# Performance work log

Measured on AMD Instinct MI355X. Metric: run time of the kernel, lower is better.

The kernel has to match this reference:

```python
import jax, jax.numpy as jnp
import numpy as np

B, S, F = 256, 192, 64
HD, L, PRED = 1024, 2, 48


def setup_inputs() -> dict:
    key = jax.random.key(0)
    ks = jax.random.split(key, 9)
    s_in = 1.0 / np.sqrt(F)
    s_h = 1.0 / np.sqrt(HD)
    return {
        "x": jax.random.normal(ks[0], (B, S, F), dtype=jnp.float32),
        "W_hidden": jax.random.uniform(ks[1], (F, HD), jnp.float32, -s_in, s_in),
        "b_hidden": jax.random.uniform(ks[2], (HD,), jnp.float32, -s_in, s_in),
        "Wih": jax.random.uniform(ks[3], (L, HD, HD), jnp.float32, -s_h, s_h),
        "Whh": jax.random.uniform(ks[4], (L, HD, HD), jnp.float32, -s_h, s_h),
        "bih": jax.random.uniform(ks[5], (L, HD), jnp.float32, -s_h, s_h),
        "bhh": jax.random.uniform(ks[6], (L, HD), jnp.float32, -s_h, s_h),
        "Wo": jax.random.uniform(ks[7], (HD, F), jnp.float32, -s_h, s_h),
        "bo": jax.random.uniform(ks[8], (F,), jnp.float32, -s_h, s_h),
    }


def reference(x, W_hidden, b_hidden, Wih, Whh, bih, bhh, Wo, bo):
    # x: [B, S, F]
    x_concat = x @ W_hidden + b_hidden          # [B, S, HD]
    xs = jnp.swapaxes(x_concat, 0, 1)           # [S, B, HD] for time scan
    h0 = jnp.zeros((L, x.shape[0], HD), x.dtype)

    def step(h, x_t):
        # h: [L, B, HD], x_t: [B, HD]; standard tanh-RNN stacked layers
        inp = x_t
        new_h = []
        for l in range(L):
            hl = jnp.tanh(inp @ Wih[l] + bih[l] + h[l] @ Whh[l] + bhh[l])
            new_h.append(hl)
            inp = hl
        h_new = jnp.stack(new_h)
        return h_new, h_new[-1]

    _, ys = jax.lax.scan(step, h0, xs)           # ys: [S, B, HD] top-layer states
    # torch code stores h for t in [0, S-2] only (drops last timestep)
    H = jnp.swapaxes(ys[:-1], 0, 1)              # [B, S-1, HD]
    H = jax.nn.relu(H)
    out = H @ Wo + bo                            # [B, S-1, F]
    return out[:, -PRED:, :]
```

## Files before the change

kernel.cpp:

```cpp
#include <hip/hip_runtime.h>
#include <hip/hip_bf16.h>

#define B    256
#define S    192
#define F    64
#define HD   1024
#define PRED 48
#define TSTART (S - 1 - PRED)
#define NSLOT 48

typedef __attribute__((ext_vector_type(8))) short short8;
typedef __attribute__((ext_vector_type(4))) float f32x4;
typedef unsigned int u32;

static __device__ __forceinline__ short f2bf(float f) {
    __hip_bfloat16 h = __float2bfloat16(f);
    return *reinterpret_cast<short*>(&h);
}
static __device__ __forceinline__ f32x4 mfma16(short8 a, short8 b, f32x4 c) {
    return __builtin_amdgcn_mfma_f32_16x16x32_bf16(a, b, c, 0, 0, 0);
}
static __device__ __forceinline__ short8 ld8(const short* p) {
    return *reinterpret_cast<const short8*>(p);
}
static __device__ __forceinline__ void st_state(short* p, short v) {
    __hip_atomic_store(p, v, __ATOMIC_RELAXED, __HIP_MEMORY_SCOPE_AGENT);
}
static __device__ __forceinline__ u32 ld_flag(const u32* p) {
    return __hip_atomic_load(p, __ATOMIC_RELAXED, __HIP_MEMORY_SCOPE_AGENT);
}
static __device__ __forceinline__ void st_flag(u32* p, u32 v) {
    __hip_atomic_store(p, v, __ATOMIC_RELAXED, __HIP_MEMORY_SCOPE_AGENT);
}

__global__ void fold_kernel(const float* __restrict__ Wh,
                            const float* __restrict__ Wih0,
                            float* __restrict__ Wfold) {
    const int n = (blockIdx.x & 3) * 256 + threadIdx.x;
    const int f = blockIdx.x >> 2;
    float a = 0.f;
#pragma unroll 16
    for (int k = 0; k < HD; ++k)
        a += Wh[f * HD + k] * Wih0[(size_t)k * HD + n];
    Wfold[f * HD + n] = a;
}

__global__ void bias_kernel(const float* __restrict__ bh,
                            const float* __restrict__ Wih0,
                            const float* __restrict__ bih,
                            const float* __restrict__ bhh,
                            float* __restrict__ bf0,
                            float* __restrict__ bf1) {
    __shared__ float red[256];
    const int nl = threadIdx.x & 15;
    const int kc = threadIdx.x >> 4;
    const int n  = blockIdx.x * 16 + nl;
    float a = 0.f;
#pragma unroll 8
    for (int k = kc * 64; k < kc * 64 + 64; ++k)
        a += bh[k] * Wih0[(size_t)k * HD + n];
    red[threadIdx.x] = a;
    __syncthreads();
    if (kc == 0) {
        float s = 0.f;
#pragma unroll
        for (int j = 0; j < 16; ++j) s += red[j * 16 + nl];
        bf0[n] = s + bih[n] + bhh[n];
        bf1[n] = bih[HD + n] + bhh[HD + n];
    }
}

__global__ void transpose_cast(const float* __restrict__ src,
                               short* __restrict__ dst, int K, int N) {
    __shared__ float tile[64][65];
    const int nk = K >> 6;
    const int bk = blockIdx.x % nk;
    const int bn = blockIdx.x / nk;
    const int i  = threadIdx.x;
    {
        const int c4 = (i & 15) * 4;
        for (int it = 0; it < 4; ++it) {
            const int k = (i >> 4) + it * 16;
            const float4 v = *reinterpret_cast<const float4*>(
                &src[(size_t)(bk * 64 + k) * N + bn * 64 + c4]);
            tile[k][c4 + 0] = v.x; tile[k][c4 + 1] = v.y;
            tile[k][c4 + 2] = v.z; tile[k][c4 + 3] = v.w;
        }
    }
    __syncthreads();
    {
        const int n  = i >> 2;
        const int kb = (i & 3) * 16;
        short* dp = &dst[(size_t)(bn * 64 + n) * K + bk * 64 + kb];
#pragma unroll
        for (int j = 0; j < 16; ++j) dp[j] = f2bf(tile[kb + j][n]);
    }
}

__global__ void xcast(const float* __restrict__ x, short* __restrict__ xb) {
    const size_t i = ((size_t)blockIdx.x * 256 + threadIdx.x) * 4;
    const float4 v = *reinterpret_cast<const float4*>(&x[i]);
    short4 o;
    o.x = f2bf(v.x); o.y = f2bf(v.y); o.z = f2bf(v.z); o.w = f2bf(v.w);
    *reinterpret_cast<short4*>(&xb[i]) = o;
}

static __device__ __forceinline__ void stage1(char* lds, const short* __restrict__ src,
                                              int row0) {
    const int tid = threadIdx.x;
#pragma unroll
    for (int it = 0; it < 8; ++it) {
        const int idx = it * 512 + tid;
        const int r   = (idx >> 2) & 31;
        const int off = ((idx >> 7) << 6) + ((idx & 3) << 4);
        const f32x4 v = *reinterpret_cast<const f32x4*>(
            (const char*)src + (size_t)(row0 + r) * 2048 + off);
        *reinterpret_cast<f32x4*>(lds + (idx << 4)) = v;
    }
}

static __device__ __forceinline__ void stage2(char* lds,
                                              const short* __restrict__ s0,
                                              const short* __restrict__ s1,
                                              int row0) {
    const int tid = threadIdx.x;
#pragma unroll
    for (int it = 0; it < 8; ++it) {
        const int idx = it * 512 + tid;
        const int r   = (idx >> 2) & 31;
        const int off = ((idx >> 7) << 6) + ((idx & 3) << 4);
        const size_t g = (size_t)(row0 + r) * 2048 + off;
        const f32x4 a = *reinterpret_cast<const f32x4*>((const char*)s0 + g);
        const f32x4 b = *reinterpret_cast<const f32x4*>((const char*)s1 + g);
        *reinterpret_cast<f32x4*>(lds + (idx << 4)) = a;
        *reinterpret_cast<f32x4*>(lds + 65536 + (idx << 4)) = b;
    }
}

static __device__ __forceinline__ f32x4 gemmLG(const char* ldsA,
                                               const short* __restrict__ bp,
                                               f32x4 acc_in) {
    f32x4 acc0 = acc_in, acc1 = {0.f,0.f,0.f,0.f};
    short8 b0[8], b1[8];
#pragma unroll
    for (int j = 0; j < 8; ++j) b0[j] = ld8(bp + j * 32);
#pragma unroll
    for (int c = 0; c < 4; ++c) {
        if (c < 3) {
            short8* nxt = (c & 1) ? b0 : b1;
#pragma unroll
            for (int j = 0; j < 8; ++j) nxt[j] = ld8(bp + (c + 1) * 256 + j * 32);
        }
        const short8* cur = (c & 1) ? b1 : b0;
#pragma unroll
        for (int j = 0; j < 8; ++j) {
            const short8 a = *reinterpret_cast<const short8*>(
                ldsA + (c * 8 + j) * 2048);
            if (j & 1) acc1 = mfma16(a, cur[j], acc1);
            else       acc0 = mfma16(a, cur[j], acc0);
        }
    }
    return acc0 + acc1;
}

__global__ __launch_bounds__(512, 1) void rnn_pers(
    const short* __restrict__ xbf,
    const short* __restrict__ WfoldT, const float* __restrict__ bf0,
    const short* __restrict__ WhhT0, const short* __restrict__ WihT1,
    const short* __restrict__ WhhT1, const float* __restrict__ bf1,
    short* h0h, short* h1h, u32* flags0, u32* flags1) {

    extern __shared__ char lds[];

    const int bid   = blockIdx.x;
    const int xcd   = bid & 7;
    const int u     = bid >> 3;
    const int layer = u & 1;
    const int rt    = ((xcd & 3) << 1) | ((u >> 1) & 1);
    const int ct    = ((xcd >> 2) << 3) | ((u >> 2) & 7);
    const int w     = threadIdx.x >> 6;
    const int mh    = w & 1;
    const int nq    = w >> 1;
    const int l     = threadIdx.x & 63;
    const int lr    = l & 15, kg = l >> 4;
    const int row0  = rt * 32;
    const int m0    = row0 + mh * 16;
    const int n0    = ct * 64 + nq * 16;
    const int col   = n0 + lr;
    const int rb    = m0 + kg * 4;
    const char* ldsA = lds + mh * 1024 + lr * 64 + kg * 16;

    const float bb = (layer ? bf1 : bf0)[col];
    u32* myflag = (layer ? flags1 : flags0) + (rt * 16 + ct) * 32;
    const int tid = threadIdx.x;

    if (layer == 0) {
        const short* wf = WfoldT + (size_t)col * F + kg * 8;
        const short8 wf0 = ld8(wf), wf1 = ld8(wf + 32);
        for (int k = 0; k < S - 1; ++k) {
            const short* xp = xbf + ((size_t)(m0 + lr) * S + k) * F + kg * 8;
            const short8 xa0 = ld8(xp);
            const short8 xa1 = ld8(xp + 32);
            if (k > 0) {
                __syncthreads();
                if (tid < 16) {
                    const u32* f = flags0 + (rt * 16 + tid) * 32;
                    while (ld_flag(f) < (u32)k) __builtin_amdgcn_s_sleep(1);
                } else if (tid < 32 && k >= 46) {
                    const u32* f = flags1 + (rt * 16 + (tid - 16)) * 32;
                    while (ld_flag(f) < (u32)(k - 45)) __builtin_amdgcn_s_sleep(1);
                }
                __syncthreads();
                stage1(lds, h0h + (size_t)((k - 1) % NSLOT) * B * HD, row0);
                __syncthreads();
            }
            f32x4 acc = {0.f, 0.f, 0.f, 0.f};
            acc = mfma16(xa0, wf0, acc);
            acc = mfma16(xa1, wf1, acc);
            if (k > 0)
                acc = gemmLG(ldsA, WhhT0 + (size_t)col * HD + kg * 8, acc);
            short* hd = h0h + (size_t)(k % NSLOT) * B * HD;
#pragma unroll
            for (int r = 0; r < 4; ++r)
                st_state(&hd[(size_t)(rb + r) * HD + col],
                         f2bf(tanhf(acc[r] + bb)));
            __syncthreads();
            if (tid == 0) st_flag(myflag, (u32)(k + 1));
        }
    } else {
        if (tid == 0) st_flag(myflag, 1u);
        for (int k = 1; k < S; ++k) {
            const int t = k - 1;
            __syncthreads();
            if (tid < 16) {
                const u32* f = flags0 + (rt * 16 + tid) * 32;
                while (ld_flag(f) < (u32)k) __builtin_amdgcn_s_sleep(1);
            } else if (tid < 32) {
                const u32* f = flags1 + (rt * 16 + (tid - 16)) * 32;
                while (ld_flag(f) < (u32)k) __builtin_amdgcn_s_sleep(1);
            }
            __syncthreads();
            const short* h0src = h0h + (size_t)((k - 1) % NSLOT) * B * HD;
            if (t > 0) {
                stage2(lds, h0src,
                       h1h + (size_t)((t - 1) % NSLOT) * B * HD, row0);
            } else {
                stage1(lds, h0src, row0);
            }
            __syncthreads();
            f32x4 acc = {0.f, 0.f, 0.f, 0.f};
            acc = gemmLG(ldsA, WihT1 + (size_t)col * HD + kg * 8, acc);
            if (t > 0)
                acc = gemmLG(ldsA + 65536, WhhT1 + (size_t)col * HD + kg * 8, acc);
#pragma unroll
            for (int r = 0; r < 4; ++r)
                st_state(&h1h[(size_t)(t % NSLOT) * B * HD
                              + (size_t)(rb + r) * HD + col],
                         f2bf(tanhf(acc[r] + bb)));
            __syncthreads();
            if (tid == 0) st_flag(myflag, (u32)(k + 1));
        }
    }
}

__global__ __launch_bounds__(256) void outgemm(
    const short* __restrict__ h1h, const short* __restrict__ WoT,
    const float* __restrict__ bo, float* __restrict__ out) {
    const int w = threadIdx.x >> 6, l = threadIdx.x & 63;
    const int lr = l & 15, kg = l >> 4;
    const int m0 = blockIdx.x * 64 + w * 16;
    const int arow = m0 + lr;
    const u32 bidx = (u32)arow / 48u;
    const u32 p    = (u32)arow % 48u;
    const u32 slot = (143u + p) % 48u;

    f32x4 acc[4] = {{0.f,0.f,0.f,0.f},{0.f,0.f,0.f,0.f},
                    {0.f,0.f,0.f,0.f},{0.f,0.f,0.f,0.f}};
    const short* ap = h1h + ((size_t)slot * B + bidx) * HD + kg * 8;
    const short* bp = WoT + (size_t)lr * HD + kg * 8;
#pragma unroll 4
    for (int k0 = 0; k0 < HD; k0 += 32) {
        short8 a = ld8(ap + k0);
#pragma unroll
        for (int j = 0; j < 8; ++j) a[j] = (a[j] < 0) ? (short)0 : a[j];
#pragma unroll
        for (int c = 0; c < 4; ++c)
            acc[c] = mfma16(a, ld8(bp + (size_t)c * 16 * HD + k0), acc[c]);
    }
    const int rb = m0 + kg * 4;
#pragma unroll
    for (int c = 0; c < 4; ++c) {
        const float bbv = bo[c * 16 + lr];
#pragma unroll
        for (int r = 0; r < 4; ++r)
            out[(size_t)(rb + r) * F + c * 16 + lr] = acc[c][r] + bbv;
    }
}

extern "C" void kernel_launch(void* const* d_in, const int* in_sizes, int n_in,
                              void* d_out, int out_size, void* d_ws, size_t ws_size,
                              hipStream_t stream) {
    const float* x   = (const float*)d_in[0];
    const float* Wh  = (const float*)d_in[1];
    const float* bh  = (const float*)d_in[2];
    const float* Wih = (const float*)d_in[3];
    const float* Whh = (const float*)d_in[4];
    const float* bih = (const float*)d_in[5];
    const float* bhh = (const float*)d_in[6];
    const float* Wo  = (const float*)d_in[7];
    const float* bo  = (const float*)d_in[8];
    float* out = (float*)d_out;

    char* p = (char*)d_ws;
    float* Wfold  = (float*)p; p += (size_t)F * HD * 4;
    float* bf0    = (float*)p; p += HD * 4;
    float* bf1    = (float*)p; p += HD * 4;
    short* WfoldT = (short*)p; p += (size_t)HD * F * 2;
    short* WhhT0  = (short*)p; p += (size_t)HD * HD * 2;
    short* WihT1  = (short*)p; p += (size_t)HD * HD * 2;
    short* WhhT1  = (short*)p; p += (size_t)HD * HD * 2;
    short* WoT    = (short*)p; p += (size_t)F * HD * 2;
    short* h0h    = (short*)p; p += (size_t)NSLOT * B * HD * 2;
    short* h1h    = (short*)p; p += (size_t)NSLOT * B * HD * 2;
    short* xbf    = (short*)p; p += (size_t)B * S * F * 2;
    u32*   sync   = (u32*)p;  p += 65536;

    hipMemsetAsync(sync, 0, 65536, stream);

    fold_kernel<<<256, 256, 0, stream>>>(Wh, Wih, Wfold);
    bias_kernel<<<64, 256, 0, stream>>>(bh, Wih, bih, bhh, bf0, bf1);
    transpose_cast<<<16, 256, 0, stream>>>(Wfold, WfoldT, F, HD);
    transpose_cast<<<256, 256, 0, stream>>>(Whh, WhhT0, HD, HD);
    transpose_cast<<<256, 256, 0, stream>>>(Wih + (size_t)HD * HD, WihT1, HD, HD);
    transpose_cast<<<256, 256, 0, stream>>>(Whh + (size_t)HD * HD, WhhT1, HD, HD);
    transpose_cast<<<16, 256, 0, stream>>>(Wo, WoT, HD, F);
    xcast<<<(B * S * F) / (256 * 4), 256, 0, stream>>>(x, xbf);

    u32* flags0 = sync;
    u32* flags1 = sync + 4096;
    void* args[] = {
        (void*)&xbf, (void*)&WfoldT, (void*)&bf0, (void*)&WhhT0,
        (void*)&WihT1, (void*)&WhhT1, (void*)&bf1,
        (void*)&h0h, (void*)&h1h, (void*)&flags0, (void*)&flags1
    };
    hipLaunchCooperativeKernel((void*)rnn_pers, dim3(256), dim3(512),
                               args, 131072, stream);

    outgemm<<<192, 256, 0, stream>>>(h1h, WoT, bo, out);
}
```

Baseline: 2.379 ms.

## Keep recurrent weights resident in registers and split layer-1 wait/stage

Each wave now loads its slice of the recurrent weight matrix (Whh) into 32 short8 registers once, before the time loop, and runs the recurrent GEMM from those registers instead of reloading weights from global memory every step. Layer 1 now waits only on layer-0 flags, stages h0 and computes the Wih product, then waits on layer-1 flags and stages h1 for the Whh product, so the Wih work overlaps the wait on peer blocks. The streamed Wih GEMM uses smaller 4-wide prefetch chunks to save registers. Launch bounds change to (512,2), which caps registers and risks spills given the large resident weight array.

```diff
diff --git a/kernel.cpp b/kernel.cpp
--- a/kernel.cpp
+++ b/kernel.cpp
@@ -119,43 +119,38 @@
     }
 }
 
-static __device__ __forceinline__ void stage2(char* lds,
-                                              const short* __restrict__ s0,
-                                              const short* __restrict__ s1,
-                                              int row0) {
-    const int tid = threadIdx.x;
-#pragma unroll
-    for (int it = 0; it < 8; ++it) {
-        const int idx = it * 512 + tid;
-        const int r   = (idx >> 2) & 31;
-        const int off = ((idx >> 7) << 6) + ((idx & 3) << 4);
-        const size_t g = (size_t)(row0 + r) * 2048 + off;
-        const f32x4 a = *reinterpret_cast<const f32x4*>((const char*)s0 + g);
-        const f32x4 b = *reinterpret_cast<const f32x4*>((const char*)s1 + g);
-        *reinterpret_cast<f32x4*>(lds + (idx << 4)) = a;
-        *reinterpret_cast<f32x4*>(lds + 65536 + (idx << 4)) = b;
-    }
-}
-
-static __device__ __forceinline__ f32x4 gemmLG(const char* ldsA,
-                                               const short* __restrict__ bp,
-                                               f32x4 acc_in) {
+static __device__ __forceinline__ f32x4 gemmR(const char* ldsA,
+                                              const short8 (&wr)[32],
+                                              f32x4 acc_in) {
     f32x4 acc0 = acc_in, acc1 = {0.f,0.f,0.f,0.f};
-    short8 b0[8], b1[8];
-#pragma unroll
-    for (int j = 0; j < 8; ++j) b0[j] = ld8(bp + j * 32);
-#pragma unroll
-    for (int c = 0; c < 4; ++c) {
-        if (c < 3) {
+#pragma unroll
+    for (int c = 0; c < 32; ++c) {
+        const short8 a = *reinterpret_cast<const short8*>(ldsA + c * 2048);
+        if (c & 1) acc1 = mfma16(a, wr[c], acc1);
+        else       acc0 = mfma16(a, wr[c], acc0);
+    }
+    return acc0 + acc1;
+}
+
+static __device__ __forceinline__ f32x4 gemmLG4(const char* ldsA,
+                                                const short* __restrict__ bp,
+                                                f32x4 acc_in) {
+    f32x4 acc0 = acc_in, acc1 = {0.f,0.f,0.f,0.f};
+    short8 b0[4], b1[4];
+#pragma unroll
+    for (int j = 0; j < 4; ++j) b0[j] = ld8(bp + j * 32);
+#pragma unroll
+    for (int c = 0; c < 8; ++c) {
+        if (c < 7) {
             short8* nxt = (c & 1) ? b0 : b1;
 #pragma unroll
-            for (int j = 0; j < 8; ++j) nxt[j] = ld8(bp + (c + 1) * 256 + j * 32);
+            for (int j = 0; j < 4; ++j) nxt[j] = ld8(bp + (c + 1) * 128 + j * 32);
         }
         const short8* cur = (c & 1) ? b1 : b0;
 #pragma unroll
-        for (int j = 0; j < 8; ++j) {
+        for (int j = 0; j < 4; ++j) {
             const short8 a = *reinterpret_cast<const short8*>(
-                ldsA + (c * 8 + j) * 2048);
+                ldsA + (c * 4 + j) * 2048);
             if (j & 1) acc1 = mfma16(a, cur[j], acc1);
             else       acc0 = mfma16(a, cur[j], acc0);
         }
@@ -163,7 +158,7 @@
     return acc0 + acc1;
 }
 
-__global__ __launch_bounds__(512, 1) void rnn_pers(
+__global__ __launch_bounds__(512, 2) void rnn_pers(
     const short* __restrict__ xbf,
     const short* __restrict__ WfoldT, const float* __restrict__ bf0,
     const short* __restrict__ WhhT0, const short* __restrict__ WihT1,
@@ -194,6 +189,13 @@
     u32* myflag = (layer ? flags1 : flags0) + (rt * 16 + ct) * 32;
     const int tid = threadIdx.x;
 
+    short8 wr[32];
+    {
+        const short* wp = (layer ? WhhT1 : WhhT0) + (size_t)col * HD + kg * 8;
+#pragma unroll
+        for (int c = 0; c < 32; ++c) wr[c] = ld8(wp + c * 32);
+    }
+
     if (layer == 0) {
         const short* wf = WfoldT + (size_t)col * F + kg * 8;
         const short8 wf0 = ld8(wf), wf1 = ld8(wf + 32);
@@ -217,8 +219,7 @@
             f32x4 acc = {0.f, 0.f, 0.f, 0.f};
             acc = mfma16(xa0, wf0, acc);
             acc = mfma16(xa1, wf1, acc);
-            if (k > 0)
-                acc = gemmLG(ldsA, WhhT0 + (size_t)col * HD + kg * 8, acc);
+            if (k > 0) acc = gemmR(ldsA, wr, acc);
             short* hd = h0h + (size_t)(k % NSLOT) * B * HD;
 #pragma unroll
             for (int r = 0; r < 4; ++r)
@@ -229,29 +230,30 @@
         }
     } else {
         if (tid == 0) st_flag(myflag, 1u);
+        char* ldsBbuf = lds + 65536;
+        const char* ldsB = ldsBbuf + mh * 1024 + lr * 64 + kg * 16;
         for (int k = 1; k < S; ++k) {
             const int t = k - 1;
             __syncthreads();
             if (tid < 16) {
                 const u32* f = flags0 + (rt * 16 + tid) * 32;
                 while (ld_flag(f) < (u32)k) __builtin_amdgcn_s_sleep(1);
-            } else if (tid < 32) {
-                const u32* f = flags1 + (rt * 16 + (tid - 16)) * 32;
-                while (ld_flag(f) < (u32)k) __builtin_amdgcn_s_sleep(1);
             }
             __syncthreads();
-            const short* h0src = h0h + (size_t)((k - 1) % NSLOT) * B * HD;
+            stage1(lds, h0h + (size_t)((k - 1) % NSLOT) * B * HD, row0);
+            __syncthreads();
+            f32x4 acc = {0.f, 0.f, 0.f, 0.f};
+            acc = gemmLG4(ldsA, WihT1 + (size_t)col * HD + kg * 8, acc);
             if (t > 0) {
-                stage2(lds, h0src,
-                       h1h + (size_t)((t - 1) % NSLOT) * B * HD, row0);
-            } else {
-                stage1(lds, h0src, row0);
+                if (tid < 16) {
+                    const u32* f = flags1 + (rt * 16 + tid) * 32;
+                    while (ld_flag(f) < (u32)k) __builtin_amdgcn_s_sleep(1);
+                }
+                __syncthreads();
+                stage1(ldsBbuf, h1h + (size_t)((t - 1) % NSLOT) * B * HD, row0);
+                __syncthreads();
+                acc = gemmR(ldsB, wr, acc);
             }
-            __syncthreads();
-            f32x4 acc = {0.f, 0.f, 0.f, 0.f};
-            acc = gemmLG(ldsA, WihT1 + (size_t)col * HD + kg * 8, acc);
-            if (t > 0)
-                acc = gemmLG(ldsA + 65536, WhhT1 + (size_t)col * HD + kg * 8, acc);
 #pragma unroll
             for (int r = 0; r < 4; ++r)
                 st_state(&h1h[(size_t)(t % NSLOT) * B * HD
```

Result: faster. 2.254 ms (-5.3%).

## Pipeline layer-1 input GEMM ahead of recurrent dependency wait

Applied to the files above, without the earlier changes.

In the layer-1 recurrence, the Wih·h0 product for the current step is computed from LDS before waiting on the layer-1 flags. The next step's layer-0 state is prefetched into registers while the Whh GEMM runs, then written into LDS after the flag is published. This takes the input projection and the next h0 load off the critical serial path between timesteps. In exchange it adds register pressure from the eight prefetch vectors and an extra barrier.

```diff
diff --git a/kernel.cpp b/kernel.cpp
--- a/kernel.cpp
+++ b/kernel.cpp
@@ -119,21 +119,25 @@
     }
 }
 
-static __device__ __forceinline__ void stage2(char* lds,
-                                              const short* __restrict__ s0,
-                                              const short* __restrict__ s1,
-                                              int row0) {
+static __device__ __forceinline__ void pre_load(f32x4 (&pre)[8],
+                                                const short* __restrict__ src,
+                                                int row0) {
     const int tid = threadIdx.x;
 #pragma unroll
     for (int it = 0; it < 8; ++it) {
         const int idx = it * 512 + tid;
         const int r   = (idx >> 2) & 31;
         const int off = ((idx >> 7) << 6) + ((idx & 3) << 4);
-        const size_t g = (size_t)(row0 + r) * 2048 + off;
-        const f32x4 a = *reinterpret_cast<const f32x4*>((const char*)s0 + g);
-        const f32x4 b = *reinterpret_cast<const f32x4*>((const char*)s1 + g);
-        *reinterpret_cast<f32x4*>(lds + (idx << 4)) = a;
-        *reinterpret_cast<f32x4*>(lds + 65536 + (idx << 4)) = b;
+        pre[it] = *reinterpret_cast<const f32x4*>(
+            (const char*)src + (size_t)(row0 + r) * 2048 + off);
+    }
+}
+static __device__ __forceinline__ void pre_write(char* lds, const f32x4 (&pre)[8]) {
+    const int tid = threadIdx.x;
+#pragma unroll
+    for (int it = 0; it < 8; ++it) {
+        const int idx = it * 512 + tid;
+        *reinterpret_cast<f32x4*>(lds + (idx << 4)) = pre[it];
     }
 }
 
@@ -197,6 +201,7 @@
     if (layer == 0) {
         const short* wf = WfoldT + (size_t)col * F + kg * 8;
         const short8 wf0 = ld8(wf), wf1 = ld8(wf + 32);
+        const short* whh0p = WhhT0 + (size_t)col * HD + kg * 8;
         for (int k = 0; k < S - 1; ++k) {
             const short* xp = xbf + ((size_t)(m0 + lr) * S + k) * F + kg * 8;
             const short8 xa0 = ld8(xp);
@@ -217,8 +222,7 @@
             f32x4 acc = {0.f, 0.f, 0.f, 0.f};
             acc = mfma16(xa0, wf0, acc);
             acc = mfma16(xa1, wf1, acc);
-            if (k > 0)
-                acc = gemmLG(ldsA, WhhT0 + (size_t)col * HD + kg * 8, acc);
+            if (k > 0) acc = gemmLG(ldsA, whh0p, acc);
             short* hd = h0h + (size_t)(k % NSLOT) * B * HD;
 #pragma unroll
             for (int r = 0; r < 4; ++r)
@@ -229,29 +233,41 @@
         }
     } else {
         if (tid == 0) st_flag(myflag, 1u);
+        char* ldsBbuf = lds + 65536;
+        const char* ldsB = ldsBbuf + mh * 1024 + lr * 64 + kg * 16;
+        const short* wih1p = WihT1 + (size_t)col * HD + kg * 8;
+        const short* whh1p = WhhT1 + (size_t)col * HD + kg * 8;
+
+        if (tid < 16) {
+            const u32* f = flags0 + (rt * 16 + tid) * 32;
+            while (ld_flag(f) < 1u) __builtin_amdgcn_s_sleep(1);
+        }
+        __syncthreads();
+        stage1(lds, h0h, row0);
+        __syncthreads();
+
         for (int k = 1; k < S; ++k) {
             const int t = k - 1;
-            __syncthreads();
+            f32x4 acc = {0.f, 0.f, 0.f, 0.f};
+            acc = gemmLG(ldsA, wih1p, acc);
             if (tid < 16) {
-                const u32* f = flags0 + (rt * 16 + tid) * 32;
-                while (ld_flag(f) < (u32)k) __builtin_amdgcn_s_sleep(1);
-            } else if (tid < 32) {
+                if (k + 1 < S) {
+                    const u32* f = flags0 + (rt * 16 + tid) * 32;
+                    while (ld_flag(f) < (u32)(k + 1)) __builtin_amdgcn_s_sleep(1);
+                }
+            } else if (tid < 32 && t > 0) {
                 const u32* f = flags1 + (rt * 16 + (tid - 16)) * 32;
                 while (ld_flag(f) < (u32)k) __builtin_amdgcn_s_sleep(1);
             }
             __syncthreads();
-            const short* h0src = h0h + (size_t)((k - 1) % NSLOT) * B * HD;
+            f32x4 pre[8];
+            if (k + 1 < S)
+                pre_load(pre, h0h + (size_t)(k % NSLOT) * B * HD, row0);
             if (t > 0) {
-                stage2(lds, h0src,
-                       h1h + (size_t)((t - 1) % NSLOT) * B * HD, row0);
-            } else {
-                stage1(lds, h0src, row0);
+                stage1(ldsBbuf, h1h + (size_t)((t - 1) % NSLOT) * B * HD, row0);
+                __syncthreads();
+                acc = gemmLG(ldsB, whh1p, acc);
             }
-            __syncthreads();
-            f32x4 acc = {0.f, 0.f, 0.f, 0.f};
-            acc = gemmLG(ldsA, WihT1 + (size_t)col * HD + kg * 8, acc);
-            if (t > 0)
-                acc = gemmLG(ldsA + 65536, WhhT1 + (size_t)col * HD + kg * 8, acc);
 #pragma unroll
             for (int r = 0; r < 4; ++r)
                 st_state(&h1h[(size_t)(t % NSLOT) * B * HD
@@ -259,6 +275,10 @@
                          f2bf(tanhf(acc[r] + bb)));
             __syncthreads();
             if (tid == 0) st_flag(myflag, (u32)(k + 1));
+            if (k + 1 < S) {
+                pre_write(lds, pre);
+                __syncthreads();
+            }
         }
     }
 }
```

Measured after the change: 2.175 ms. 8.6% less time.
